# Kernel optimization log

Hardware: AMD Instinct MI355X
Metric: run time of the kernel (lower is better)

Reference implementation:

```python
import jax, jax.numpy as jnp
import numpy as np

H = 768
NH = 12
HD = H // NH


def setup_inputs() -> dict:
    key = jax.random.key(0)
    ks = jax.random.split(key, 12)
    B, S = 2, 2048
    s = 1.0 / np.sqrt(H)
    inp = {
        "hidden_states": jax.random.normal(ks[0], (B, S, H), dtype=jnp.float32),
        "attention_mask": jnp.ones((B, S), dtype=jnp.float32),
        "Wq": jax.random.normal(ks[1], (H, H), dtype=jnp.float32) * s,
        "bq": jnp.zeros((H,), dtype=jnp.float32),
        "Wk": jax.random.normal(ks[2], (H, H), dtype=jnp.float32) * s,
        "bk": jnp.zeros((H,), dtype=jnp.float32),
        "Wv": jax.random.normal(ks[3], (H, H), dtype=jnp.float32) * s,
        "bv": jnp.zeros((H,), dtype=jnp.float32),
        "Wo": jax.random.normal(ks[4], (H, H), dtype=jnp.float32) * s,
        "bo": jnp.zeros((H,), dtype=jnp.float32),
        "ln_gamma": jnp.ones((H,), dtype=jnp.float32),
        "ln_beta": jnp.zeros((H,), dtype=jnp.float32),
    }
    return inp


def _split_heads(x):
    # [B,S,H] -> [B,NH,S,HD]
    B, S, _ = x.shape
    return x.reshape(B, S, NH, HD).transpose(0, 2, 1, 3)


def reference(hidden_states, attention_mask, Wq, bq, Wk, bk, Wv, bv, Wo, bo, ln_gamma, ln_beta):
    x = hidden_states
    q = _split_heads(x @ Wq.T + bq)
    k = _split_heads(x @ Wk.T + bk)
    v = _split_heads(x @ Wv.T + bv)
    # scores: [B,NH,S,S]
    scores = jnp.einsum("bhqd,bhkd->bhqk", q, k) / jnp.sqrt(jnp.float32(HD))
    mask = (1.0 - attention_mask)[:, None, None, :] * -10000.0
    scores = scores + mask
    probs = jax.nn.softmax(scores, axis=-1)  # dropout is identity at inference
    ctx = jnp.einsum("bhqk,bhkd->bhqd", probs, v)
    B, _, S, _ = ctx.shape
    ctx = ctx.transpose(0, 2, 1, 3).reshape(B, S, H)
    out = ctx @ Wo.T + bo
    y = out + x
    mu = jnp.mean(y, axis=-1, keepdims=True)
    var = jnp.var(y, axis=-1, keepdims=True)
    y = (y - mu) / jnp.sqrt(var + 1e-5)
    return y * ln_gamma + ln_beta
```

## Files before the change

kernel.cpp:

```cpp
#include <hip/hip_runtime.h>
#include <math.h>

#define HH 768
#define NHEADS 12
#define HDIM 64
#define SEQ 2048
#define NB 2
#define L2E 1.44269504088896f

typedef __attribute__((ext_vector_type(8))) short s8v;
typedef __attribute__((ext_vector_type(4))) short s4v;
typedef __attribute__((ext_vector_type(4))) float f4v;

static __device__ inline short f2bf(float f) {
    union { float f; unsigned u; } v; v.f = f;
    unsigned r = v.u + 0x7fff + ((v.u >> 16) & 1);
    return (short)(r >> 16);
}

#if __has_builtin(__builtin_amdgcn_exp2f)
#define EXP2(x) __builtin_amdgcn_exp2f(x)
#else
#define EXP2(x) __expf((x) * 0.6931471805599453f)
#endif

__device__ __forceinline__ unsigned cvt_pk_bf16(float a, float b) {
    unsigned r;
    asm("v_cvt_pk_bf16_f32 %0, %1, %2" : "=v"(r) : "v"(a), "v"(b));
    return r;
}

__device__ __forceinline__ void gld16(const void* g, void* l) {
    __builtin_amdgcn_global_load_lds(
        (const __attribute__((address_space(1))) void*)g,
        (__attribute__((address_space(3))) void*)l, 16, 0, 0);
}

#define XV8   393216
#define WV8   73728
__global__ __launch_bounds__(256)
void cvt_kernel(const float* __restrict__ X, short* __restrict__ Xb,
                const float* __restrict__ W0, short* __restrict__ W0b,
                const float* __restrict__ W1, short* __restrict__ W1b,
                const float* __restrict__ W2, short* __restrict__ W2b,
                const float* __restrict__ W3, short* __restrict__ W3b)
{
    int gid = blockIdx.x * 256 + threadIdx.x;
    const float* src; short* dst; size_t off;
    if      (gid < XV8)            { src = X;  dst = Xb;  off = gid; }
    else if (gid < XV8 + WV8)      { src = W0; dst = W0b; off = gid - XV8; }
    else if (gid < XV8 + 2*WV8)    { src = W1; dst = W1b; off = gid - XV8 - WV8; }
    else if (gid < XV8 + 3*WV8)    { src = W2; dst = W2b; off = gid - XV8 - 2*WV8; }
    else if (gid < XV8 + 4*WV8)    { src = W3; dst = W3b; off = gid - XV8 - 3*WV8; }
    else return;
    off *= 8;
    float4 a = *(const float4*)(src + off);
    float4 b = *(const float4*)(src + off + 4);
    s8v o;
    o[0] = f2bf(a.x); o[1] = f2bf(a.y); o[2] = f2bf(a.z); o[3] = f2bf(a.w);
    o[4] = f2bf(b.x); o[5] = f2bf(b.y); o[6] = f2bf(b.z); o[7] = f2bf(b.w);
    *(s8v*)(dst + off) = o;
}

template<int EPI>
__global__ __launch_bounds__(256)
void gemm_mfma(const short* __restrict__ A,
               const short* __restrict__ Wq, const short* __restrict__ Wk,
               const short* __restrict__ Wv,
               const float* __restrict__ bq, const float* __restrict__ bk,
               const float* __restrict__ bv,
               short* __restrict__ Qo, short* __restrict__ Ko, short* __restrict__ Vo,
               const float* __restrict__ Xres, float* __restrict__ Fo)
{
    __shared__ __align__(16) short As[128*32];
    __shared__ __align__(16) short Bs[128*32];

    const int tid  = threadIdx.x;
    const int w    = tid >> 6;
    const int lane = tid & 63;
    const int g    = lane >> 4;
    const int r    = lane & 15;
    const int wr   = w >> 1;
    const int wc   = w & 1;
    const int m0   = blockIdx.y * 128;

    int n0;
    int seg = 0;
    const short* Wb; const float* bias; short* outp; float scale;
    if (EPI == 0) {
        seg = blockIdx.x / 6;
        n0 = (blockIdx.x % 6) * 128;
        Wb   = seg == 0 ? Wq : seg == 1 ? Wk : Wv;
        bias = seg == 0 ? bq : seg == 1 ? bk : bv;
        outp = seg == 0 ? Qo : seg == 1 ? Ko : Vo;
        scale = seg == 0 ? (0.125f * L2E) : 1.0f;
    } else {
        n0 = blockIdx.x * 128;
        Wb = Wq; bias = bq; outp = nullptr; scale = 1.0f;
    }

    const int lrow = lane >> 2;
    const int lcol = (lane & 3) * 8;
    const short* Ag0 = A  + (size_t)(m0 + w*32 + lrow) * HH + lcol;
    const short* Bg0 = Wb + (size_t)(n0 + w*32 + lrow) * HH + lcol;
    short* Al0 = As + (w*32)      * 32;
    short* Al1 = As + (w*32 + 16) * 32;
    short* Bl0 = Bs + (w*32)      * 32;
    short* Bl1 = Bs + (w*32 + 16) * 32;

    f4v acc[4][4];
    #pragma unroll
    for (int i = 0; i < 4; i++)
        #pragma unroll
        for (int j = 0; j < 4; j++) acc[i][j] = (f4v){0.f,0.f,0.f,0.f};

    for (int kt = 0; kt < HH/32; ++kt) {
        const int k0 = kt * 32;
        gld16(Ag0 + k0,           Al0);
        gld16(Ag0 + k0 + 16*HH,   Al1);
        gld16(Bg0 + k0,           Bl0);
        gld16(Bg0 + k0 + 16*HH,   Bl1);
        __syncthreads();

        s8v af[4], bf[4];
        #pragma unroll
        for (int mi = 0; mi < 4; mi++)
            af[mi] = *(const s8v*)(As + (wr*64 + mi*16 + r)*32 + g*8);
        #pragma unroll
        for (int ni = 0; ni < 4; ni++)
            bf[ni] = *(const s8v*)(Bs + (wc*64 + ni*16 + r)*32 + g*8);
        __builtin_amdgcn_s_setprio(1);
        #pragma unroll
        for (int mi = 0; mi < 4; mi++)
            #pragma unroll
            for (int ni = 0; ni < 4; ni++)
                acc[mi][ni] = __builtin_amdgcn_mfma_f32_16x16x32_bf16(af[mi], bf[ni], acc[mi][ni], 0, 0, 0);
        __builtin_amdgcn_s_setprio(0);
        __syncthreads();
    }

    if (EPI == 0) {
        if (seg < 2) {
            #pragma unroll
            for (int mi = 0; mi < 4; mi++) {
                #pragma unroll
                for (int j = 0; j < 4; j++) {
                    const int m = m0 + wr*64 + mi*16 + 4*g + j;
                    const int bb = m >> 11;
                    const int s  = m & 2047;
                    #pragma unroll
                    for (int ni = 0; ni < 4; ni++) {
                        const int n = n0 + wc*64 + ni*16 + r;
                        const int h = n >> 6;
                        const int d = n & 63;
                        outp[((size_t)((bb*NHEADS + h)*SEQ) + s)*HDIM + d] =
                            f2bf((acc[mi][ni][j] + bias[n]) * scale);
                    }
                }
            }
        } else {
            #pragma unroll
            for (int mi = 0; mi < 4; mi++) {
                const int m  = m0 + wr*64 + mi*16 + 4*g;
                const int bb = m >> 11;
                const int s  = m & 2047;
                #pragma unroll
                for (int ni = 0; ni < 4; ni++) {
                    const int n = n0 + wc*64 + ni*16 + r;
                    const int h = n >> 6;
                    const int d = n & 63;
                    s4v pk;
                    #pragma unroll
                    for (int j = 0; j < 4; j++)
                        pk[j] = f2bf(acc[mi][ni][j] + bias[n]);
                    *(s4v*)(outp + ((size_t)((bb*NHEADS + h)*HDIM) + d)*SEQ + s) = pk;
                }
            }
        }
    } else {
        #pragma unroll
        for (int mi = 0; mi < 4; mi++) {
            #pragma unroll
            for (int j = 0; j < 4; j++) {
                const int m = m0 + wr*64 + mi*16 + 4*g + j;
                #pragma unroll
                for (int ni = 0; ni < 4; ni++) {
                    const int n = n0 + wc*64 + ni*16 + r;
                    Fo[(size_t)m*HH + n] = acc[mi][ni][j] + bias[n] + Xres[(size_t)m*HH + n];
                }
            }
        }
    }
}

#define NPAIR (SEQ/64)
__global__ __launch_bounds__(512, 4)
void attn_mfma(const short* __restrict__ Q, const short* __restrict__ K,
               const short* __restrict__ VT, const float* __restrict__ mask,
               short* __restrict__ CTX)
{
    const int wgid = (blockIdx.x & 7) * 96 + (blockIdx.x >> 3);
    const int qt = wgid & 31;
    const int bh = wgid >> 5;
    const int h  = bh % NHEADS;
    const int b  = bh / NHEADS;

    const size_t hb = (size_t)(b * NHEADS + h);
    const short* Qg  = Q  + hb * SEQ * HDIM;
    const short* Kg  = K  + hb * SEQ * HDIM;
    const short* VTg = VT + hb * HDIM * SEQ;

    __shared__ __align__(16) char lds[53248];
    char* Kbase = lds;
    char* Vbase = lds + 16384;
    char* Pbase = lds + 32768;
    short* Mls  = (short*)(lds + 49152);

    const int tid  = threadIdx.x;
    const int w    = tid >> 6;
    const int grp  = w >> 2;
    const int wq   = w & 3;
    const int lane = tid & 63;
    const int g    = lane >> 4;
    const int r    = lane & 15;
    const int q0   = qt * 64;

    const short* qrow = Qg + (size_t)(q0 + wq*16 + r) * HDIM;
    const s8v qf0 = *(const s8v*)(qrow + 8*g);
    const s8v qf1 = *(const s8v*)(qrow + 8*g + 32);

    {
        float4 mv = *(const float4*)(mask + b*SEQ + tid*4);
        s4v md;
        md[0] = f2bf((mv.x - 1.0f) * (10000.0f * L2E));
        md[1] = f2bf((mv.y - 1.0f) * (10000.0f * L2E));
        md[2] = f2bf((mv.z - 1.0f) * (10000.0f * L2E));
        md[3] = f2bf((mv.w - 1.0f) * (10000.0f * L2E));
        *(s4v*)(Mls + tid*4) = md;
    }

    f4v acc[4];
    #pragma unroll
    for (int t = 0; t < 4; t++) acc[t] = (f4v){0.f, 0.f, 0.f, 0.f};
    f4v lsum = (f4v){0.f, 0.f, 0.f, 0.f};

    const int srow = lane >> 3;
    const int scol = 8 * ((lane & 7) ^ srow);

    #define STAGE(PT, DB) do {                                                 \
        const int pk0 = (PT) * 64;                                             \
        char* kd = Kbase + (DB)*8192 + w*1024;                                 \
        gld16(Kg + (size_t)(pk0 + 8*w + srow)*HDIM + scol, kd);                \
        char* vd = Vbase + (DB)*8192 + w*1024;                                 \
        gld16(VTg + (size_t)(8*w + srow)*SEQ + pk0 + scol, vd);                \
    } while (0)

    STAGE(0, 0);
    __syncthreads();

    char* pb = Pbase + w*2048;

    for (int pt = 0; pt < NPAIR; ++pt) {
        const int db = pt & 1;
        if (pt + 1 < NPAIR) STAGE(pt + 1, db ^ 1);

        const char* Kc = Kbase + db*8192 + grp*4096;
        const char* Vc = Vbase + db*8192;
        const int k0 = pt*64 + grp*32;

        float madd[2];
        {
            union { unsigned u; float f; } c0, c1;
            c0.u = ((unsigned)(unsigned short)Mls[k0 + r])      << 16;
            c1.u = ((unsigned)(unsigned short)Mls[k0 + 16 + r]) << 16;
            madd[0] = c0.f;
            madd[1] = c1.f;
        }

        f4v sj[2];
        __builtin_amdgcn_s_setprio(1);
        #pragma unroll
        for (int j = 0; j < 2; j++) {
            const int krow = 16*j + r;
            const char* kb = Kc + krow * 128;
            const int sw = (r & 7) << 4;
            s8v kf0 = *(const s8v*)(kb + ((16*g)      ^ sw));
            s8v kf1 = *(const s8v*)(kb + ((16*g + 64) ^ sw));
            f4v z = (f4v){0.f, 0.f, 0.f, 0.f};
            z = __builtin_amdgcn_mfma_f32_16x16x32_bf16(qf0, kf0, z, 0, 0, 0);
            z = __builtin_amdgcn_mfma_f32_16x16x32_bf16(qf1, kf1, z, 0, 0, 0);
            #pragma unroll
            for (int i = 0; i < 4; i++) z[i] += madd[j];
            sj[j] = z;
        }
        __builtin_amdgcn_s_setprio(0);

        #pragma unroll
        for (int j = 0; j < 2; j++)
            #pragma unroll
            for (int i = 0; i < 4; i++)
                sj[j][i] = EXP2(sj[j][i]);
        #pragma unroll
        for (int i = 0; i < 4; i++)
            lsum[i] += sj[0][i] + sj[1][i];

        #pragma unroll
        for (int i = 0; i < 4; i++) {
            const int prow = 4*g + i;
            char* base = pb + prow * 128;
            const int sw = (prow & 7) << 4;
            unsigned u = cvt_pk_bf16(sj[0][i], sj[1][i]);
            *(short*)(base + ((r*2)        ^ sw)) = (short)(u & 0xffff);
            *(short*)(base + ((32 + r*2)   ^ sw)) = (short)(u >> 16);
        }

        __builtin_amdgcn_s_setprio(1);
        {
            s8v pf = *(const s8v*)(pb + r*128 + ((16*g) ^ ((r & 7) << 4)));
            #pragma unroll
            for (int t4 = 0; t4 < 4; t4++) {
                const int vrow = 16*t4 + r;
                s8v vf = *(const s8v*)(Vc + vrow*128 + ((16*(4*grp + g)) ^ ((r & 7) << 4)));
                acc[t4] = __builtin_amdgcn_mfma_f32_16x16x32_bf16(pf, vf, acc[t4], 0, 0, 0);
            }
        }
        __builtin_amdgcn_s_setprio(0);

        __syncthreads();
    }

    if (grp == 1) {
        float* mb = (float*)(lds + wq*5120 + lane*80);
        *(f4v*)(mb)      = acc[0];
        *(f4v*)(mb + 4)  = acc[1];
        *(f4v*)(mb + 8)  = acc[2];
        *(f4v*)(mb + 12) = acc[3];
        *(f4v*)(mb + 16) = lsum;
    }
    __syncthreads();
    if (grp == 0) {
        const float* mb = (const float*)(lds + wq*5120 + lane*80);
        acc[0] += *(const f4v*)(mb);
        acc[1] += *(const f4v*)(mb + 4);
        acc[2] += *(const f4v*)(mb + 8);
        acc[3] += *(const f4v*)(mb + 12);
        lsum   += *(const f4v*)(mb + 16);

        #pragma unroll
        for (int m = 1; m <= 8; m <<= 1) {
            lsum[0] += __shfl_xor(lsum[0], m);
            lsum[1] += __shfl_xor(lsum[1], m);
            lsum[2] += __shfl_xor(lsum[2], m);
            lsum[3] += __shfl_xor(lsum[3], m);
        }

        #pragma unroll
        for (int i = 0; i < 4; i++) {
            const float invl = 1.0f / lsum[i];
            const size_t rowbase = ((size_t)(b*SEQ) + q0 + wq*16 + 4*g + i) * HH + h*HDIM;
            #pragma unroll
            for (int t4 = 0; t4 < 4; t4++)
                CTX[rowbase + 16*t4 + r] = f2bf(acc[t4][i] * invl);
        }
    }
    #undef STAGE
}

__global__ __launch_bounds__(256)
void ln_kernel(float* __restrict__ y, const float* __restrict__ gamma,
               const float* __restrict__ beta)
{
    const int row = blockIdx.x;
    float* p = y + (size_t)row * HH;
    const int tid = threadIdx.x;

    float v[3];
    float s = 0.f, ss = 0.f;
    #pragma unroll
    for (int i = 0; i < 3; i++) {
        float x = p[tid + i*256];
        v[i] = x;
        s += x;
        ss += x * x;
    }
    #pragma unroll
    for (int off = 32; off > 0; off >>= 1) {
        s  += __shfl_down(s,  off);
        ss += __shfl_down(ss, off);
    }
    __shared__ float sbuf[4], ssbuf[4];
    __shared__ float mu_s, rstd_s;
    const int wave = tid >> 6;
    if ((tid & 63) == 0) { sbuf[wave] = s; ssbuf[wave] = ss; }
    __syncthreads();
    if (tid == 0) {
        float S  = sbuf[0] + sbuf[1] + sbuf[2] + sbuf[3];
        float SS = ssbuf[0] + ssbuf[1] + ssbuf[2] + ssbuf[3];
        float mu = S * (1.0f / HH);
        float var = SS * (1.0f / HH) - mu * mu;
        mu_s = mu;
        rstd_s = rsqrtf(var + 1e-5f);
    }
    __syncthreads();
    const float mu = mu_s, rstd = rstd_s;
    #pragma unroll
    for (int i = 0; i < 3; i++) {
        const int c = tid + i*256;
        p[c] = (v[i] - mu) * rstd * gamma[c] + beta[c];
    }
}

extern "C" void kernel_launch(void* const* d_in, const int* in_sizes, int n_in,
                              void* d_out, int out_size, void* d_ws, size_t ws_size,
                              hipStream_t stream)
{
    const float* x     = (const float*)d_in[0];
    const float* mask  = (const float*)d_in[1];
    const float* Wq    = (const float*)d_in[2];
    const float* bq    = (const float*)d_in[3];
    const float* Wk    = (const float*)d_in[4];
    const float* bk    = (const float*)d_in[5];
    const float* Wv    = (const float*)d_in[6];
    const float* bv    = (const float*)d_in[7];
    const float* Wo    = (const float*)d_in[8];
    const float* bo    = (const float*)d_in[9];
    const float* gamma = (const float*)d_in[10];
    const float* beta  = (const float*)d_in[11];

    const size_t PER = (size_t)NB * NHEADS * SEQ * HDIM;
    const size_t WSZ = (size_t)HH * HH;
    short* wsS  = (short*)d_ws;
    short* Xb   = wsS;
    short* Wqb  = wsS + PER;
    short* Wkb  = Wqb + WSZ;
    short* Wvb  = Wkb + WSZ;
    short* Wob  = Wvb + WSZ;
    short* Qb   = Wob + WSZ;
    short* Kb   = Qb + PER;
    short* VTb  = Kb + PER;
    short* CTXb = Xb;
    float* out  = (float*)d_out;

    cvt_kernel<<<2688, 256, 0, stream>>>(x, Xb, Wq, Wqb, Wk, Wkb, Wv, Wvb, Wo, Wob);

    gemm_mfma<0><<<dim3(18, 32), 256, 0, stream>>>(
        Xb, Wqb, Wkb, Wvb, bq, bk, bv, Qb, Kb, VTb, nullptr, nullptr);

    attn_mfma<<<768, 512, 0, stream>>>(Qb, Kb, VTb, mask, CTXb);

    gemm_mfma<1><<<dim3(6, 32), 256, 0, stream>>>(
        CTXb, Wob, nullptr, nullptr, bo, nullptr, nullptr,
        nullptr, nullptr, nullptr, x, out);

    ln_kernel<<<NB*SEQ, 256, 0, stream>>>(out, gamma, beta);
}
```

Before: 121.3 us.

## Compute transposed scores in registers and permute V columns to skip LDS P round-trip

The attention kernel now computes S^T (K as the A operand, Q as B), so each lane's score accumulators already match the bf16 A-fragment layout needed for the P·V MFMA after packing. This removes the per-iteration write of probabilities to shared memory and the read back. To make the key ordering line up, the V-transpose projection epilogue and the mask table store keys in a permuted order (kperm). Row sums become per-lane partials reduced by shuffles at the end. The LDS footprint drops, which may allow more resident workgroups, but correctness depends on the permutation exactly matching the MFMA register layout.

```diff
diff --git a/kernel.cpp b/kernel.cpp
--- a/kernel.cpp
+++ b/kernel.cpp
@@ -34,6 +34,10 @@
     __builtin_amdgcn_global_load_lds(
         (const __attribute__((address_space(1))) void*)g,
         (__attribute__((address_space(3))) void*)l, 16, 0, 0);
+}
+
+__device__ __forceinline__ int kperm(int k) {
+    return (k & ~31) | (((k >> 2) & 3) << 3) | (((k >> 4) & 1) << 2) | (k & 3);
 }
 
 #define XV8   393216
@@ -164,6 +168,7 @@
                 const int m  = m0 + wr*64 + mi*16 + 4*g;
                 const int bb = m >> 11;
                 const int s  = m & 2047;
+                const int sp = kperm(s);
                 #pragma unroll
                 for (int ni = 0; ni < 4; ni++) {
                     const int n = n0 + wc*64 + ni*16 + r;
@@ -173,7 +178,7 @@
                     #pragma unroll
                     for (int j = 0; j < 4; j++)
                         pk[j] = f2bf(acc[mi][ni][j] + bias[n]);
-                    *(s4v*)(outp + ((size_t)((bb*NHEADS + h)*HDIM) + d)*SEQ + s) = pk;
+                    *(s4v*)(outp + ((size_t)((bb*NHEADS + h)*HDIM) + d)*SEQ + sp) = pk;
                 }
             }
         }
@@ -210,11 +215,10 @@
     const short* Kg  = K  + hb * SEQ * HDIM;
     const short* VTg = VT + hb * HDIM * SEQ;
 
-    __shared__ __align__(16) char lds[53248];
+    __shared__ __align__(16) char lds[36864];
     char* Kbase = lds;
     char* Vbase = lds + 16384;
-    char* Pbase = lds + 32768;
-    short* Mls  = (short*)(lds + 49152);
+    short* Mper = (short*)(lds + 32768);
 
     const int tid  = threadIdx.x;
     const int w    = tid >> 6;
@@ -236,13 +240,13 @@
         md[1] = f2bf((mv.y - 1.0f) * (10000.0f * L2E));
         md[2] = f2bf((mv.z - 1.0f) * (10000.0f * L2E));
         md[3] = f2bf((mv.w - 1.0f) * (10000.0f * L2E));
-        *(s4v*)(Mls + tid*4) = md;
+        *(s4v*)(Mper + kperm(tid*4)) = md;
     }
 
     f4v acc[4];
     #pragma unroll
     for (int t = 0; t < 4; t++) acc[t] = (f4v){0.f, 0.f, 0.f, 0.f};
-    f4v lsum = (f4v){0.f, 0.f, 0.f, 0.f};
+    float lpart = 0.0f;
 
     const int srow = lane >> 3;
     const int scol = 8 * ((lane & 7) ^ srow);
@@ -258,84 +262,76 @@
     STAGE(0, 0);
     __syncthreads();
 
-    char* pb = Pbase + w*2048;
-
     for (int pt = 0; pt < NPAIR; ++pt) {
         const int db = pt & 1;
         if (pt + 1 < NPAIR) STAGE(pt + 1, db ^ 1);
 
         const char* Kc = Kbase + db*8192 + grp*4096;
         const char* Vc = Vbase + db*8192;
-        const int k0 = pt*64 + grp*32;
-
-        float madd[2];
-        {
-            union { unsigned u; float f; } c0, c1;
-            c0.u = ((unsigned)(unsigned short)Mls[k0 + r])      << 16;
-            c1.u = ((unsigned)(unsigned short)Mls[k0 + 16 + r]) << 16;
-            madd[0] = c0.f;
-            madd[1] = c1.f;
-        }
-
-        f4v sj[2];
-        __builtin_amdgcn_s_setprio(1);
-        #pragma unroll
-        for (int j = 0; j < 2; j++) {
-            const int krow = 16*j + r;
-            const char* kb = Kc + krow * 128;
-            const int sw = (r & 7) << 4;
-            s8v kf0 = *(const s8v*)(kb + ((16*g)      ^ sw));
-            s8v kf1 = *(const s8v*)(kb + ((16*g + 64) ^ sw));
-            f4v z = (f4v){0.f, 0.f, 0.f, 0.f};
-            z = __builtin_amdgcn_mfma_f32_16x16x32_bf16(qf0, kf0, z, 0, 0, 0);
-            z = __builtin_amdgcn_mfma_f32_16x16x32_bf16(qf1, kf1, z, 0, 0, 0);
-            #pragma unroll
-            for (int i = 0; i < 4; i++) z[i] += madd[j];
-            sj[j] = z;
-        }
-        __builtin_amdgcn_s_setprio(0);
-
-        #pragma unroll
-        for (int j = 0; j < 2; j++)
-            #pragma unroll
-            for (int i = 0; i < 4; i++)
-                sj[j][i] = EXP2(sj[j][i]);
-        #pragma unroll
-        for (int i = 0; i < 4; i++)
-            lsum[i] += sj[0][i] + sj[1][i];
-
-        #pragma unroll
-        for (int i = 0; i < 4; i++) {
-            const int prow = 4*g + i;
-            char* base = pb + prow * 128;
-            const int sw = (prow & 7) << 4;
-            unsigned u = cvt_pk_bf16(sj[0][i], sj[1][i]);
-            *(short*)(base + ((r*2)        ^ sw)) = (short)(u & 0xffff);
-            *(short*)(base + ((32 + r*2)   ^ sw)) = (short)(u >> 16);
-        }
-
+
+        s8v mraw = *(const s8v*)(Mper + pt*64 + grp*32 + 8*g);
+
+        f4v p0, p1;
         __builtin_amdgcn_s_setprio(1);
         {
-            s8v pf = *(const s8v*)(pb + r*128 + ((16*g) ^ ((r & 7) << 4)));
-            #pragma unroll
-            for (int t4 = 0; t4 < 4; t4++) {
-                const int vrow = 16*t4 + r;
-                s8v vf = *(const s8v*)(Vc + vrow*128 + ((16*(4*grp + g)) ^ ((r & 7) << 4)));
-                acc[t4] = __builtin_amdgcn_mfma_f32_16x16x32_bf16(pf, vf, acc[t4], 0, 0, 0);
-            }
+            const int sw = (r & 7) << 4;
+            const char* kb0 = Kc + r * 128;
+            const char* kb1 = Kc + (16 + r) * 128;
+            s8v ka0 = *(const s8v*)(kb0 + ((16*g)      ^ sw));
+            s8v ka1 = *(const s8v*)(kb0 + ((16*g + 64) ^ sw));
+            s8v kb0f = *(const s8v*)(kb1 + ((16*g)      ^ sw));
+            s8v kb1f = *(const s8v*)(kb1 + ((16*g + 64) ^ sw));
+            f4v z0 = (f4v){0.f, 0.f, 0.f, 0.f};
+            z0 = __builtin_amdgcn_mfma_f32_16x16x32_bf16(ka0, qf0, z0, 0, 0, 0);
+            z0 = __builtin_amdgcn_mfma_f32_16x16x32_bf16(ka1, qf1, z0, 0, 0, 0);
+            f4v z1 = (f4v){0.f, 0.f, 0.f, 0.f};
+            z1 = __builtin_amdgcn_mfma_f32_16x16x32_bf16(kb0f, qf0, z1, 0, 0, 0);
+            z1 = __builtin_amdgcn_mfma_f32_16x16x32_bf16(kb1f, qf1, z1, 0, 0, 0);
+            p0 = z0; p1 = z1;
         }
         __builtin_amdgcn_s_setprio(0);
 
+        #pragma unroll
+        for (int i = 0; i < 4; i++) {
+            union { unsigned u; float f; } m0c, m1c;
+            m0c.u = ((unsigned)(unsigned short)mraw[i])     << 16;
+            m1c.u = ((unsigned)(unsigned short)mraw[4 + i]) << 16;
+            p0[i] = EXP2(p0[i] + m0c.f);
+            p1[i] = EXP2(p1[i] + m1c.f);
+        }
+        lpart += ((p0[0] + p0[1]) + (p0[2] + p0[3]))
+               + ((p1[0] + p1[1]) + (p1[2] + p1[3]));
+
+        union { unsigned u[4]; s8v v; } pfu;
+        pfu.u[0] = cvt_pk_bf16(p0[0], p0[1]);
+        pfu.u[1] = cvt_pk_bf16(p0[2], p0[3]);
+        pfu.u[2] = cvt_pk_bf16(p1[0], p1[1]);
+        pfu.u[3] = cvt_pk_bf16(p1[2], p1[3]);
+        const s8v pf = pfu.v;
+
+        __builtin_amdgcn_s_setprio(1);
+        #pragma unroll
+        for (int t4 = 0; t4 < 4; t4++) {
+            const int vrow = 16*t4 + r;
+            s8v vf = *(const s8v*)(Vc + vrow*128 + ((16*(4*grp + g)) ^ ((r & 7) << 4)));
+            acc[t4] = __builtin_amdgcn_mfma_f32_16x16x32_bf16(pf, vf, acc[t4], 0, 0, 0);
+        }
+        __builtin_amdgcn_s_setprio(0);
+
         __syncthreads();
     }
 
+    lpart += __shfl_xor(lpart, 16);
+    lpart += __shfl_xor(lpart, 32);
+
+    float* lbuf = (float*)(lds + 20480);
     if (grp == 1) {
         float* mb = (float*)(lds + wq*5120 + lane*80);
         *(f4v*)(mb)      = acc[0];
         *(f4v*)(mb + 4)  = acc[1];
         *(f4v*)(mb + 8)  = acc[2];
         *(f4v*)(mb + 12) = acc[3];
-        *(f4v*)(mb + 16) = lsum;
+        lbuf[wq*64 + lane] = lpart;
     }
     __syncthreads();
     if (grp == 0) {
@@ -344,19 +340,11 @@
         acc[1] += *(const f4v*)(mb + 4);
         acc[2] += *(const f4v*)(mb + 8);
         acc[3] += *(const f4v*)(mb + 12);
-        lsum   += *(const f4v*)(mb + 16);
-
-        #pragma unroll
-        for (int m = 1; m <= 8; m <<= 1) {
-            lsum[0] += __shfl_xor(lsum[0], m);
-            lsum[1] += __shfl_xor(lsum[1], m);
-            lsum[2] += __shfl_xor(lsum[2], m);
-            lsum[3] += __shfl_xor(lsum[3], m);
-        }
+        lpart  += lbuf[wq*64 + lane];
 
         #pragma unroll
         for (int i = 0; i < 4; i++) {
-            const float invl = 1.0f / lsum[i];
+            const float invl = 1.0f / __shfl(lpart, 4*g + i);
             const size_t rowbase = ((size_t)(b*SEQ) + q0 + wq*16 + 4*g + i) * HH + h*HDIM;
             #pragma unroll
             for (int t4 = 0; t4 < 4; t4++)
```

New measurement: 111.4 us. 8.2% less time.
